# Performance work log

Hardware: AMD Instinct MI355X
Metric: run time of the kernel (lower is better)

## Reference

```python
import jax, jax.numpy as jnp
import numpy as np

# --- configuration (from init_kwargs / chosen production scale) ---
NUM_STEPS = 18
SIGMA_MIN = 0.002
SIGMA_MAX = 80.0
RHO = 7.0
CE_SIGMA = 0.2
SIGMA_DATA = 0.5  # standard EDM preconditioning constant for the surrogate net
N_CES = 2
B, C, H, W = 64, 3, 64, 64
NUM_CLASSES = 1000


def _t_steps():
    # Karras sigma schedule, computed in float64 numpy then cast (original uses fp64).
    i = np.arange(NUM_STEPS, dtype=np.float64)
    ts = (SIGMA_MAX ** (1.0 / RHO) + i / (NUM_STEPS - 1) * (SIGMA_MIN ** (1.0 / RHO) - SIGMA_MAX ** (1.0 / RHO))) ** RHO
    ts = np.concatenate([ts, np.zeros(1)])  # append t_N = 0 (net.round_sigma ~ identity)
    return jnp.asarray(ts, dtype=jnp.float32)


def _net(x, sigma, W_net, b_net):
    # EDM-preconditioned denoiser surrogate: D(x) = c_skip*x + c_out*F(c_in*x)
    s2 = sigma * sigma
    denom = s2 + SIGMA_DATA ** 2
    c_skip = SIGMA_DATA ** 2 / denom
    c_out = sigma * SIGMA_DATA * jax.lax.rsqrt(denom)
    c_in = jax.lax.rsqrt(denom)
    f = jax.lax.conv_general_dilated(c_in * x, W_net, (1, 1), 'SAME',
                                     dimension_numbers=('NCHW', 'OIHW', 'NCHW'))
    f = f + b_net[None, :, None, None]
    return c_skip * x + c_out * f


def _sample(mu_ce, latents, noise, W_net, b_net):
    # EDM Euler ODE/SDE sampler with counterfactual drift toward mu_ce.
    ts = _t_steps()  # [NUM_STEPS+1]
    x0 = latents * ts[0]

    def step(x_cur, inp):
        t_cur, t_next, eps = inp
        denoised = _net(x_cur, t_cur, W_net, b_net)
        dx_dt = (denoised - x_cur) / t_cur + t_cur * (mu_ce - x_cur) / (CE_SIGMA ** 2 + t_cur * t_cur)
        # eps is pre-zeroed for the last two steps (i >= NUM_STEPS-2)
        x_next = x_cur + 2.0 * dx_dt * (t_cur - t_next) + jnp.sqrt(2.0 * t_cur * (t_cur - t_next)) * eps
        return x_next, None

    x_final, _ = jax.lax.scan(step, x0, (ts[:-1], ts[1:], noise))
    return x_final


def setup_inputs() -> dict:
    key = jax.random.key(0)
    k_x, k_lat, k_noise, k_wn, k_wc = jax.random.split(key, 5)
    x = jax.random.uniform(k_x, (B, C, H, W), dtype=jnp.float32)  # images in [0,1]
    latents = jax.random.normal(k_lat, (N_CES * B, C, H, W), dtype=jnp.float32)
    noise = jax.random.normal(k_noise, (NUM_STEPS, N_CES * B, C, H, W), dtype=jnp.float32)
    # noise is only injected for i < NUM_STEPS - 2
    mask = (jnp.arange(NUM_STEPS) < NUM_STEPS - 2).astype(jnp.float32)
    noise = noise * mask[:, None, None, None, None]
    W_net = 0.05 * jax.random.normal(k_wn, (C, C, 3, 3), dtype=jnp.float32)  # OIHW
    b_net = jnp.zeros((C,), dtype=jnp.float32)
    W_cls = 0.02 * jax.random.normal(k_wc, (C * H * W, NUM_CLASSES), dtype=jnp.float32)
    b_cls = jnp.zeros((NUM_CLASSES,), dtype=jnp.float32)
    return {"x": x, "latents": latents, "noise": noise,
            "W_net": W_net, "b_net": b_net, "W_cls": W_cls, "b_cls": b_cls}


def reference(x, latents, noise, W_net, b_net, W_cls, b_cls):
    xt = jnp.tile(x, (N_CES, 1, 1, 1))          # [n_ces*B, C, H, W]
    mu_ce = 2.0 * xt - 1.0                      # rescale to [-1, 1]
    x_ces = (_sample(mu_ce, latents, noise, W_net, b_net) + 1.0) / 2.0
    logits = x_ces.reshape(N_CES * B, -1) @ W_cls + b_cls  # cls surrogate
    logits = jax.nn.logsumexp(logits.reshape(N_CES, B, NUM_CLASSES), axis=0) - jnp.log(float(N_CES))
    return logits
```

## Files before the change

kernel.cpp:

```cpp
#include <hip/hip_runtime.h>
#include <math.h>

#define NSTEPS 18
#define NS 128
#define CHW 12288
#define HW 4096
#define NCLS 1000
#define NLOC 6
#define WIN 28
#define BUFF6 (3 * WIN * 64)

struct StepC { float c_skip, c_out, c_in, inv_t, ce, two_dt, nc, pad; };
struct Steps { StepC s[NSTEPS]; float t0; };

typedef __attribute__((ext_vector_type(8))) short v8s;
typedef __attribute__((ext_vector_type(4))) float v4f;

__device__ __forceinline__ unsigned short f2bf(float f) {
    unsigned int u = __float_as_uint(f);
    unsigned int r = (u + 0x7FFFu + ((u >> 16) & 1u)) >> 16;
    return (unsigned short)r;
}

__global__ __launch_bounds__(448, 2)
void sampler6_kernel(const float* __restrict__ src, float inscale,
                     const float* __restrict__ x, const float* __restrict__ noise,
                     const float* __restrict__ Wn_g, const float* __restrict__ bn_g,
                     float* __restrict__ Xout, unsigned short* __restrict__ Aout,
                     Steps S, int s0)
{
    __shared__ float xs[2 * BUFF6];
    __shared__ float Wl[3 * 32 + 4];
    const int tid = threadIdx.x;
    const int n = blockIdx.x >> 2;
    const int q = blockIdx.x & 3;
    const int base = q << 4;
    const int w0 = (base - NLOC > 0) ? base - NLOC : 0;
    const int w1 = (base + 16 + NLOC < 64) ? base + 16 + NLOC : 64;
    const int wsize = w1 - w0;

    if (tid < 81) {
        const int co = tid / 27, r = tid % 27;
        const int ci = r / 9, r2 = r % 9;
        Wl[ci * 32 + co * 9 + r2] = Wn_g[tid];
    } else if (tid < 84) {
        Wl[96 + (tid - 81)] = bn_g[tid - 81];
    }

    const int lr = tid >> 4;
    const int cg = tid & 15;
    const int col = cg << 2;
    const int gr = w0 + lr;
    const bool rowv = (lr < wsize);

    const float* sb = src + (size_t)n * CHW;
    const float* xin = x + (size_t)(n & 63) * CHW;

    float xc[3][4], mu[3][4];
    if (rowv) {
        #pragma unroll
        for (int ci = 0; ci < 3; ++ci) {
            float4 v = *reinterpret_cast<const float4*>(sb + ci * HW + gr * 64 + col);
            v.x *= inscale; v.y *= inscale; v.z *= inscale; v.w *= inscale;
            xc[ci][0]=v.x; xc[ci][1]=v.y; xc[ci][2]=v.z; xc[ci][3]=v.w;
            *reinterpret_cast<float4*>(&xs[(ci * WIN + lr) * 64 + col]) = v;
            float4 m = *reinterpret_cast<const float4*>(xin + ci * HW + gr * 64 + col);
            mu[ci][0] = 2.f*m.x - 1.f; mu[ci][1] = 2.f*m.y - 1.f;
            mu[ci][2] = 2.f*m.z - 1.f; mu[ci][3] = 2.f*m.w - 1.f;
        }
    }
    __syncthreads();

    int cur = 0;
    for (int ls = 0; ls < NLOC; ++ls) {
        const StepC c = S.s[s0 + ls];
        const int gstep = s0 + ls;
        const int rad = NLOC - 1 - ls;
        const bool active = rowv && (gr >= base - rad) && (gr < base + 16 + rad);

        if (active) {
            float4 e0, e1, e2;
            e0 = make_float4(0.f,0.f,0.f,0.f); e1 = e0; e2 = e0;
            if (gstep < NSTEPS - 2) {
                const float* nz = noise + ((size_t)(gstep * NS + n)) * CHW + gr * 64 + col;
                e0 = *reinterpret_cast<const float4*>(nz);
                e1 = *reinterpret_cast<const float4*>(nz + HW);
                e2 = *reinterpret_cast<const float4*>(nz + 2 * HW);
            }

            float acc[3][4];
            #pragma unroll
            for (int co = 0; co < 3; ++co)
                #pragma unroll
                for (int j = 0; j < 4; ++j) acc[co][j] = 0.f;

            #pragma unroll
            for (int ci = 0; ci < 3; ++ci) {
                float wf[28];
                #pragma unroll
                for (int t = 0; t < 7; ++t) {
                    float4 wv = *reinterpret_cast<const float4*>(&Wl[ci * 32 + t * 4]);
                    wf[t*4+0] = wv.x; wf[t*4+1] = wv.y; wf[t*4+2] = wv.z; wf[t*4+3] = wv.w;
                }

                float in0[6], in2[6], cen[6];
                const float* bcur = &xs[cur * BUFF6 + ci * (WIN * 64)];
                if (gr >= 1) {
                    const float* rp = bcur + (lr - 1) * 64 + col;
                    float4 a = *reinterpret_cast<const float4*>(rp);
                    in0[1]=a.x; in0[2]=a.y; in0[3]=a.z; in0[4]=a.w;
                    in0[0] = (cg > 0)  ? rp[-1] : 0.f;
                    in0[5] = (cg < 15) ? rp[4]  : 0.f;
                } else {
                    #pragma unroll
                    for (int p = 0; p < 6; ++p) in0[p] = 0.f;
                }
                if (gr + 1 < 64) {
                    const float* rp = bcur + (lr + 1) * 64 + col;
                    float4 a = *reinterpret_cast<const float4*>(rp);
                    in2[1]=a.x; in2[2]=a.y; in2[3]=a.z; in2[4]=a.w;
                    in2[0] = (cg > 0)  ? rp[-1] : 0.f;
                    in2[5] = (cg < 15) ? rp[4]  : 0.f;
                } else {
                    #pragma unroll
                    for (int p = 0; p < 6; ++p) in2[p] = 0.f;
                }
                {
                    const float* rp = bcur + lr * 64 + col;
                    cen[0] = (cg > 0)  ? rp[-1] : 0.f;
                    cen[5] = (cg < 15) ? rp[4]  : 0.f;
                    #pragma unroll
                    for (int j = 0; j < 4; ++j) cen[j + 1] = xc[ci][j];
                }

                #pragma unroll
                for (int co = 0; co < 3; ++co) {
                    #pragma unroll
                    for (int dw = 0; dw < 3; ++dw) {
                        const float w0t = wf[co * 9 + dw];
                        const float w1t = wf[co * 9 + 3 + dw];
                        const float w2t = wf[co * 9 + 6 + dw];
                        #pragma unroll
                        for (int j = 0; j < 4; ++j) {
                            acc[co][j] = fmaf(w0t, in0[j + dw],
                                         fmaf(w1t, cen[j + dw],
                                         fmaf(w2t, in2[j + dw], acc[co][j])));
                        }
                    }
                }
            }

            const float bn0 = Wl[96], bn1 = Wl[97], bn2 = Wl[98];
            const float eps[3][4] = {{e0.x,e0.y,e0.z,e0.w},
                                     {e1.x,e1.y,e1.z,e1.w},
                                     {e2.x,e2.y,e2.z,e2.w}};
            const float bnv[3] = {bn0, bn1, bn2};
            #pragma unroll
            for (int co = 0; co < 3; ++co) {
                #pragma unroll
                for (int j = 0; j < 4; ++j) {
                    const float xv = xc[co][j];
                    const float f = fmaf(c.c_in, acc[co][j], bnv[co]);
                    const float den = c.c_skip * xv + c.c_out * f;
                    const float dx = (den - xv) * c.inv_t + c.ce * (mu[co][j] - xv);
                    xc[co][j] = fmaf(c.two_dt, dx, fmaf(c.nc, eps[co][j], xv));
                }
            }
            #pragma unroll
            for (int co = 0; co < 3; ++co)
                *reinterpret_cast<float4*>(&xs[(cur ^ 1) * BUFF6 + (co * WIN + lr) * 64 + col]) =
                    make_float4(xc[co][0], xc[co][1], xc[co][2], xc[co][3]);
        }
        __syncthreads();
        cur ^= 1;
    }

    if (rowv && gr >= base && gr < base + 16) {
        if (s0 + NLOC >= NSTEPS) {
            unsigned short* Ao = Aout + (size_t)n * CHW;
            #pragma unroll
            for (int ci = 0; ci < 3; ++ci) {
                ushort4 o;
                o.x = f2bf((xc[ci][0] + 1.f) * 0.5f); o.y = f2bf((xc[ci][1] + 1.f) * 0.5f);
                o.z = f2bf((xc[ci][2] + 1.f) * 0.5f); o.w = f2bf((xc[ci][3] + 1.f) * 0.5f);
                *reinterpret_cast<ushort4*>(Ao + ci * HW + gr * 64 + col) = o;
            }
        } else {
            float* Xo = Xout + (size_t)n * CHW;
            #pragma unroll
            for (int ci = 0; ci < 3; ++ci)
                *reinterpret_cast<float4*>(Xo + ci * HW + gr * 64 + col) =
                    make_float4(xc[ci][0], xc[ci][1], xc[ci][2], xc[ci][3]);
        }
    }
}

__global__ __launch_bounds__(256)
void gemm_kernel(const unsigned short* __restrict__ Abf, const float* __restrict__ Wc,
                 float* __restrict__ part, int bkc)
{
    const int tid = threadIdx.x;
    const int wv = tid >> 6;
    const int lane = tid & 63;
    const int lrow = lane & 15;
    const int lk8 = (lane >> 4) << 3;
    const int ct = blockIdx.x & 15;
    const int kc = blockIdx.x >> 4;
    const int c0 = ct << 6;
    const int k0 = kc * bkc;

    v4f acc[2][4];
    #pragma unroll
    for (int rt = 0; rt < 2; ++rt)
        #pragma unroll
        for (int c4 = 0; c4 < 4; ++c4) acc[rt][c4] = (v4f)0.f;

    #pragma unroll 2
    for (int kk = 0; kk < bkc; kk += 32) {
        const int kb = k0 + kk + lk8;
        v8s a[2];
        #pragma unroll
        for (int rt = 0; rt < 2; ++rt)
            a[rt] = *reinterpret_cast<const v8s*>(Abf + (size_t)(wv * 32 + rt * 16 + lrow) * CHW + kb);
        v8s b[4];
        #pragma unroll
        for (int c4 = 0; c4 < 4; ++c4) {
            const int col = c0 + c4 * 16 + lrow;
            const bool cv = (col < NCLS);
            #pragma unroll
            for (int j = 0; j < 8; ++j) {
                const float f = cv ? Wc[(size_t)(kb + j) * NCLS + col] : 0.f;
                b[c4][j] = (short)f2bf(f);
            }
        }
        #pragma unroll
        for (int rt = 0; rt < 2; ++rt)
            #pragma unroll
            for (int c4 = 0; c4 < 4; ++c4)
                acc[rt][c4] = __builtin_amdgcn_mfma_f32_16x16x32_bf16(a[rt], b[c4], acc[rt][c4], 0, 0, 0);
    }

    float* pp = part + (size_t)kc * NS * NCLS;
    #pragma unroll
    for (int rt = 0; rt < 2; ++rt)
        #pragma unroll
        for (int c4 = 0; c4 < 4; ++c4) {
            const int col = c0 + c4 * 16 + lrow;
            if (col < NCLS) {
                #pragma unroll
                for (int r = 0; r < 4; ++r) {
                    const int row = wv * 32 + rt * 16 + (lane >> 4) * 4 + r;
                    pp[(size_t)row * NCLS + col] = acc[rt][c4][r];
                }
            }
        }
}

__global__ __launch_bounds__(256)
void lse_kernel(const float* __restrict__ part, const float* __restrict__ bcls,
                float* __restrict__ out, int ks)
{
    const int i = blockIdx.x * 256 + threadIdx.x;
    if (i >= 64 * NCLS) return;
    const int b = i / NCLS;
    const int k = i - b * NCLS;
    float l0 = bcls[k], l1 = bcls[k];
    for (int kc = 0; kc < ks; ++kc) {
        l0 += part[(size_t)kc * NS * NCLS + (size_t)b * NCLS + k];
        l1 += part[(size_t)kc * NS * NCLS + (size_t)(b + 64) * NCLS + k];
    }
    const float m = fmaxf(l0, l1);
    out[i] = m + logf(expf(l0 - m) + expf(l1 - m)) - 0.69314718055994530942f;
}

extern "C" void kernel_launch(void* const* d_in, const int* in_sizes, int n_in,
                              void* d_out, int out_size, void* d_ws, size_t ws_size,
                              hipStream_t stream) {
    const float* x       = (const float*)d_in[0];
    const float* latents = (const float*)d_in[1];
    const float* noise   = (const float*)d_in[2];
    const float* W_net   = (const float*)d_in[3];
    const float* b_net   = (const float*)d_in[4];
    const float* W_cls   = (const float*)d_in[5];
    const float* b_cls   = (const float*)d_in[6];
    float* out = (float*)d_out;

    float* XA = (float*)d_ws;
    float* XB = XA + (size_t)NS * CHW;
    unsigned short* Amat = (unsigned short*)(XB + (size_t)NS * CHW);
    const size_t head_bytes = (size_t)NS * CHW * 4 * 2 + (size_t)NS * CHW * 2;
    float* part = (float*)((char*)d_ws + head_bytes);

    Steps S;
    const double smin = pow(0.002, 1.0 / 7.0), smax = pow(80.0, 1.0 / 7.0);
    float tsf[NSTEPS + 1];
    for (int i = 0; i < NSTEPS; ++i) {
        double v = smax + (double)i / (double)(NSTEPS - 1) * (smin - smax);
        tsf[i] = (float)pow(v, 7.0);
    }
    tsf[NSTEPS] = 0.f;
    S.t0 = tsf[0];
    for (int i = 0; i < NSTEPS; ++i) {
        const float t = tsf[i], tn = tsf[i + 1];
        const float s2 = t * t, denom = s2 + 0.25f;
        StepC c;
        c.c_skip = 0.25f / denom;
        c.c_out  = t * 0.5f / sqrtf(denom);
        c.c_in   = 1.0f / sqrtf(denom);
        c.inv_t  = 1.0f / t;
        c.ce     = t / (0.04f + s2);
        const float dt = t - tn;
        c.two_dt = 2.f * dt;
        c.nc     = sqrtf(2.f * t * dt);
        c.pad    = 0.f;
        S.s[i] = c;
    }

    int KS = 32;
    while (KS > 1 && head_bytes + (size_t)KS * NS * NCLS * 4 > ws_size) KS >>= 1;
    const int bkc = CHW / KS;

    sampler6_kernel<<<NS * 4, 448, 0, stream>>>(latents, S.t0, x, noise, W_net, b_net, XA, Amat, S, 0);
    sampler6_kernel<<<NS * 4, 448, 0, stream>>>(XA, 1.f, x, noise, W_net, b_net, XB, Amat, S, 6);
    sampler6_kernel<<<NS * 4, 448, 0, stream>>>(XB, 1.f, x, noise, W_net, b_net, XB, Amat, S, 12);
    gemm_kernel<<<16 * KS, 256, 0, stream>>>(Amat, W_cls, part, bkc);
    lse_kernel<<<(64 * NCLS + 255) / 256, 256, 0, stream>>>(part, b_cls, out, KS);
}
```

Before: 120.7 us.

## Stage W_cls tiles in shared memory with coalesced float4 loads in classifier GEMM

The classifier GEMM now loads each 32x64 tile of W_cls with coalesced float4 reads, converts it to bf16 once into a shared-memory tile, and all four waves read their B fragments from LDS. Before, every wave gathered strided scalar fp32 values per lane and converted them separately, so each W element was fetched four times. The K split is also fixed at 16 at compile time instead of being sized from the workspace, which halves the block count and the partial sums the reduction reads. The cost is two barriers per K step, a padded LDS tile, and no check that the workspace is large enough.

Measured after the change: 124.7 us. +3.3%, slower.

```diff
diff --git a/kernel.cpp b/kernel.cpp
--- a/kernel.cpp
+++ b/kernel.cpp
@@ -9,6 +9,8 @@
 #define NLOC 6
 #define WIN 28
 #define BUFF6 (3 * WIN * 64)
+#define KSPLIT 16
+#define BKC (CHW / KSPLIT)
 
 struct StepC { float c_skip, c_out, c_in, inv_t, ce, two_dt, nc, pad; };
 struct Steps { StepC s[NSTEPS]; float t0; };
@@ -197,8 +199,9 @@
 
 __global__ __launch_bounds__(256)
 void gemm_kernel(const unsigned short* __restrict__ Abf, const float* __restrict__ Wc,
-                 float* __restrict__ part, int bkc)
+                 float* __restrict__ part)
 {
+    __shared__ unsigned short Bs[64][40];
     const int tid = threadIdx.x;
     const int wv = tid >> 6;
     const int lane = tid & 63;
@@ -207,7 +210,7 @@
     const int ct = blockIdx.x & 15;
     const int kc = blockIdx.x >> 4;
     const int c0 = ct << 6;
-    const int k0 = kc * bkc;
+    const int k0 = kc * BKC;
 
     v4f acc[2][4];
     #pragma unroll
@@ -215,29 +218,43 @@
         #pragma unroll
         for (int c4 = 0; c4 < 4; ++c4) acc[rt][c4] = (v4f)0.f;
 
-    #pragma unroll 2
-    for (int kk = 0; kk < bkc; kk += 32) {
-        const int kb = k0 + kk + lk8;
+    const int skrow = tid >> 4;
+    const int scc  = (tid & 15) << 2;
+
+    for (int kk = 0; kk < BKC; kk += 32) {
+        const int kb = k0 + kk;
+        #pragma unroll
+        for (int p = 0; p < 2; ++p) {
+            const int kr = skrow + p * 16;
+            const int gc = c0 + scc;
+            float4 v = make_float4(0.f, 0.f, 0.f, 0.f);
+            if (gc + 3 < NCLS) {
+                v = *reinterpret_cast<const float4*>(Wc + (size_t)(kb + kr) * NCLS + gc);
+            } else if (gc < NCLS) {
+                const float* wp = Wc + (size_t)(kb + kr) * NCLS;
+                v.x = wp[gc];
+                v.y = (gc + 1 < NCLS) ? wp[gc + 1] : 0.f;
+                v.z = (gc + 2 < NCLS) ? wp[gc + 2] : 0.f;
+            }
+            Bs[scc + 0][kr] = f2bf(v.x);
+            Bs[scc + 1][kr] = f2bf(v.y);
+            Bs[scc + 2][kr] = f2bf(v.z);
+            Bs[scc + 3][kr] = f2bf(v.w);
+        }
+        __syncthreads();
+
         v8s a[2];
         #pragma unroll
         for (int rt = 0; rt < 2; ++rt)
-            a[rt] = *reinterpret_cast<const v8s*>(Abf + (size_t)(wv * 32 + rt * 16 + lrow) * CHW + kb);
-        v8s b[4];
+            a[rt] = *reinterpret_cast<const v8s*>(Abf + (size_t)(wv * 32 + rt * 16 + lrow) * CHW + kb + lk8);
         #pragma unroll
         for (int c4 = 0; c4 < 4; ++c4) {
-            const int col = c0 + c4 * 16 + lrow;
-            const bool cv = (col < NCLS);
-            #pragma unroll
-            for (int j = 0; j < 8; ++j) {
-                const float f = cv ? Wc[(size_t)(kb + j) * NCLS + col] : 0.f;
-                b[c4][j] = (short)f2bf(f);
-            }
-        }
-        #pragma unroll
-        for (int rt = 0; rt < 2; ++rt)
-            #pragma unroll
-            for (int c4 = 0; c4 < 4; ++c4)
-                acc[rt][c4] = __builtin_amdgcn_mfma_f32_16x16x32_bf16(a[rt], b[c4], acc[rt][c4], 0, 0, 0);
+            const v8s b = *reinterpret_cast<const v8s*>(&Bs[c4 * 16 + lrow][lk8]);
+            #pragma unroll
+            for (int rt = 0; rt < 2; ++rt)
+                acc[rt][c4] = __builtin_amdgcn_mfma_f32_16x16x32_bf16(a[rt], b, acc[rt][c4], 0, 0, 0);
+        }
+        __syncthreads();
     }
 
     float* pp = part + (size_t)kc * NS * NCLS;
@@ -258,14 +275,15 @@
 
 __global__ __launch_bounds__(256)
 void lse_kernel(const float* __restrict__ part, const float* __restrict__ bcls,
-                float* __restrict__ out, int ks)
+                float* __restrict__ out)
 {
     const int i = blockIdx.x * 256 + threadIdx.x;
     if (i >= 64 * NCLS) return;
     const int b = i / NCLS;
     const int k = i - b * NCLS;
     float l0 = bcls[k], l1 = bcls[k];
-    for (int kc = 0; kc < ks; ++kc) {
+    #pragma unroll 4
+    for (int kc = 0; kc < KSPLIT; ++kc) {
         l0 += part[(size_t)kc * NS * NCLS + (size_t)b * NCLS + k];
         l1 += part[(size_t)kc * NS * NCLS + (size_t)(b + 64) * NCLS + k];
     }
@@ -316,13 +334,9 @@
         S.s[i] = c;
     }
 
-    int KS = 32;
-    while (KS > 1 && head_bytes + (size_t)KS * NS * NCLS * 4 > ws_size) KS >>= 1;
-    const int bkc = CHW / KS;
-
     sampler6_kernel<<<NS * 4, 448, 0, stream>>>(latents, S.t0, x, noise, W_net, b_net, XA, Amat, S, 0);
     sampler6_kernel<<<NS * 4, 448, 0, stream>>>(XA, 1.f, x, noise, W_net, b_net, XB, Amat, S, 6);
     sampler6_kernel<<<NS * 4, 448, 0, stream>>>(XB, 1.f, x, noise, W_net, b_net, XB, Amat, S, 12);
-    gemm_kernel<<<16 * KS, 256, 0, stream>>>(Amat, W_cls, part, bkc);
-    lse_kernel<<<(64 * NCLS + 255) / 256, 256, 0, stream>>>(part, b_cls, out, KS);
-}
+    gemm_kernel<<<16 * KSPLIT, 256, 0, stream>>>(Amat, W_cls, part);
+    lse_kernel<<<(64 * NCLS + 255) / 256, 256, 0, stream>>>(part, b_cls, out);
+}
```
